# Optimization experiments

Hardware: AMD Instinct MI355X
Metric: run time of the kernel (lower is better)

The kernel has to match this reference:

```python
import jax, jax.numpy as jnp
import numpy as np

N_NODES = 5000
N_EDGES = 40000
BATCH = 4
SEQ = 12
IN_FEAT = 64
OUT_FEAT = 64


def setup_inputs() -> dict:
    key = jax.random.key(0)
    k1, k2, k3, k4 = jax.random.split(key, 4)
    features = jax.random.normal(k1, (N_NODES, BATCH, SEQ, IN_FEAT), dtype=jnp.float32)
    # glorot-uniform-like scale for the shared weight
    limit = np.sqrt(6.0 / (IN_FEAT + OUT_FEAT)).astype(np.float32)
    weight = jax.random.uniform(k2, (IN_FEAT, OUT_FEAT), dtype=jnp.float32,
                                minval=-limit, maxval=limit)
    edges_dst = jax.random.randint(k3, (N_EDGES,), 0, N_NODES, dtype=jnp.int32)
    edges_src = jax.random.randint(k4, (N_EDGES,), 0, N_NODES, dtype=jnp.int32)
    return {"features": features, "weight": weight,
            "edges_dst": edges_dst, "edges_src": edges_src}


def reference(features, weight, edges_dst, edges_src):
    num_nodes = features.shape[0]
    # nodes' own representation: (N, B, T, Fin) @ (Fin, Fout)
    nodes_rep = jnp.matmul(features, weight)
    # gather source-node features for every edge: (E, B, T, Fin)
    gathered = features[edges_src]
    # unsorted_segment_mean over destination nodes
    summed = jax.ops.segment_sum(gathered, edges_dst, num_segments=num_nodes)
    counts = jax.ops.segment_sum(jnp.ones((edges_dst.shape[0],), dtype=features.dtype),
                                 edges_dst, num_segments=num_nodes)
    mean = summed / jnp.maximum(counts, 1.0)[:, None, None, None]
    agg_messages = jnp.matmul(mean, weight)
    # combination_type = 'concat', activation = relu
    h = jnp.concatenate([nodes_rep, agg_messages], axis=-1)
    return jax.nn.relu(h)
```

## Files before the change

kernel.cpp:

```cpp
#include <hip/hip_runtime.h>

#define N_NODES 5000
#define N_EDGES 40000
#define ROWS 48
#define FIN 64
#define FOUT 64
#define NODE_ELEMS (ROWS * FIN)
#define OUT_ROW 128
#define NODE_OUT (ROWS * OUT_ROW)
#define CAP 64
#define M_ROWS (N_NODES * ROWS)

typedef float f32x4 __attribute__((ext_vector_type(4)));
typedef short bf16x8 __attribute__((ext_vector_type(8)));

__device__ __forceinline__ unsigned short f32_to_bf16_rne(float f) {
    unsigned int u = __float_as_uint(f);
    u += 0x7fffu + ((u >> 16) & 1u);
    return (unsigned short)(u >> 16);
}


__global__ void prep_kernel(const float* __restrict__ W,
                            int* __restrict__ counts,
                            unsigned short* __restrict__ Wt) {
    const int tid = threadIdx.x;
    if (blockIdx.x < 20) {
        int i = blockIdx.x * 256 + tid;
        if (i < N_NODES) counts[i] = 0;
    } else {
        int base = tid * 16;
        int j = base >> 6;
        int k0 = base & 63;
        ushort4 pk[4];
        #pragma unroll
        for (int q = 0; q < 4; ++q) {
            unsigned short p[4];
            #pragma unroll
            for (int m = 0; m < 4; ++m)
                p[m] = f32_to_bf16_rne(W[(k0 + q * 4 + m) * 64 + j]);
            pk[q].x = p[0]; pk[q].y = p[1]; pk[q].z = p[2]; pk[q].w = p[3];
        }
        #pragma unroll
        for (int q = 0; q < 4; ++q)
            *(ushort4*)(Wt + j * 64 + k0 + q * 4) = pk[q];
    }
}

__global__ void bucket_kernel(const int* __restrict__ edges_dst,
                              const int* __restrict__ edges_src,
                              int* __restrict__ counts,
                              int* __restrict__ bucket) {
    int e = blockIdx.x * 256 + threadIdx.x;
    if (e < N_EDGES) {
        int d = edges_dst[e];
        int slot = atomicAdd(&counts[d], 1);
        if (slot < CAP) bucket[d * CAP + slot] = edges_src[e];
    }
}


__global__ __launch_bounds__(256) void mfma_matmul_kernel(
    const float* __restrict__ feat,
    const unsigned short* __restrict__ Wt,
    float* __restrict__ out,
    unsigned short* __restrict__ Q) {
    __shared__ __align__(16) float c_lds[64 * 64];

    const int tid  = threadIdx.x;
    const int wave = tid >> 6;
    const int lane = tid & 63;
    const int row16 = lane & 15;
    const int koct  = lane >> 4;

    const size_t g0 = (size_t)blockIdx.x * 64;

    const float* arow = feat + (g0 + wave * 16 + row16) * FIN + koct * 8;
    f32x4 a00 = *(const f32x4*)(arow);
    f32x4 a01 = *(const f32x4*)(arow + 4);
    f32x4 a10 = *(const f32x4*)(arow + 32);
    f32x4 a11 = *(const f32x4*)(arow + 36);

    bf16x8 bfrag[2][4];
    #pragma unroll
    for (int t = 0; t < 4; ++t) {
        const unsigned short* wcol = Wt + (t * 16 + row16) * 64 + koct * 8;
        bfrag[0][t] = *(const bf16x8*)(wcol);
        bfrag[1][t] = *(const bf16x8*)(wcol + 32);
    }

    bf16x8 afrag[2];
    {
        unsigned short p[16];
        #pragma unroll
        for (int m = 0; m < 4; ++m) {
            p[m]      = f32_to_bf16_rne(a00[m]);
            p[4 + m]  = f32_to_bf16_rne(a01[m]);
            p[8 + m]  = f32_to_bf16_rne(a10[m]);
            p[12 + m] = f32_to_bf16_rne(a11[m]);
        }
        #pragma unroll
        for (int m = 0; m < 8; ++m) { afrag[0][m] = (short)p[m]; afrag[1][m] = (short)p[8 + m]; }
    }

    f32x4 acc[4];
    #pragma unroll
    for (int t = 0; t < 4; ++t) acc[t] = (f32x4){0.f, 0.f, 0.f, 0.f};

    #pragma unroll
    for (int s = 0; s < 2; ++s)
        #pragma unroll
        for (int t = 0; t < 4; ++t)
            acc[t] = __builtin_amdgcn_mfma_f32_16x16x32_bf16(afrag[s], bfrag[s][t], acc[t], 0, 0, 0);

    #pragma unroll
    for (int t = 0; t < 4; ++t)
        #pragma unroll
        for (int p = 0; p < 4; ++p)
            c_lds[(wave * 16 + koct * 4 + p) * 64 + t * 16 + row16] = acc[t][p];
    __syncthreads();

    #pragma unroll
    for (int i = 0; i < 4; ++i) {
        int c = tid + i * 256;
        int r = c >> 4;
        int cq = c & 15;
        f32x4 v = ((const f32x4*)c_lds)[c];
        f32x4 rv = {fmaxf(v.x, 0.f), fmaxf(v.y, 0.f), fmaxf(v.z, 0.f), fmaxf(v.w, 0.f)};
        *(f32x4*)(out + (g0 + r) * OUT_ROW + cq * 4) = rv;
    }
    #pragma unroll
    for (int i = 0; i < 2; ++i) {
        int c = tid + i * 256;
        int r = c >> 3;
        int part = c & 7;
        const float* src = c_lds + r * 64 + part * 8;
        ushort4 lo, hi;
        lo.x = f32_to_bf16_rne(src[0]); lo.y = f32_to_bf16_rne(src[1]);
        lo.z = f32_to_bf16_rne(src[2]); lo.w = f32_to_bf16_rne(src[3]);
        hi.x = f32_to_bf16_rne(src[4]); hi.y = f32_to_bf16_rne(src[5]);
        hi.z = f32_to_bf16_rne(src[6]); hi.w = f32_to_bf16_rne(src[7]);
        unsigned short* dst = Q + (g0 + r) * FIN + part * 8;
        *(ushort4*)(dst) = lo;
        *(ushort4*)(dst + 4) = hi;
    }
}


__device__ __forceinline__ void acc_u4(float* a, uint4 v) {
    a[0] += __uint_as_float(v.x << 16); a[1] += __uint_as_float(v.x & 0xffff0000u);
    a[2] += __uint_as_float(v.y << 16); a[3] += __uint_as_float(v.y & 0xffff0000u);
    a[4] += __uint_as_float(v.z << 16); a[5] += __uint_as_float(v.z & 0xffff0000u);
    a[6] += __uint_as_float(v.w << 16); a[7] += __uint_as_float(v.w & 0xffff0000u);
}

__global__ __launch_bounds__(384) void gather_kernel(
    const unsigned short* __restrict__ Q,
    const int* __restrict__ counts,
    const int* __restrict__ bucket,
    float* __restrict__ out) {
    const int n = blockIdx.x;
    const int tid = threadIdx.x;
    const int cnt_true = counts[n];
    const int cnt = cnt_true < CAP ? cnt_true : CAP;
    const int* bk = bucket + n * CAP;

    float acc[8];
    #pragma unroll
    for (int i = 0; i < 8; ++i) acc[i] = 0.f;

    int e = 0;
    for (; e + 4 <= cnt; e += 4) {
        const unsigned short* q0 = Q + (size_t)bk[e]     * NODE_ELEMS;
        const unsigned short* q1 = Q + (size_t)bk[e + 1] * NODE_ELEMS;
        const unsigned short* q2 = Q + (size_t)bk[e + 2] * NODE_ELEMS;
        const unsigned short* q3 = Q + (size_t)bk[e + 3] * NODE_ELEMS;
        uint4 a0 = *(const uint4*)(q0 + tid * 8);
        uint4 a1 = *(const uint4*)(q1 + tid * 8);
        uint4 a2 = *(const uint4*)(q2 + tid * 8);
        uint4 a3 = *(const uint4*)(q3 + tid * 8);
        acc_u4(acc, a0); acc_u4(acc, a1); acc_u4(acc, a2); acc_u4(acc, a3);
    }
    for (; e < cnt; ++e) {
        const unsigned short* q0 = Q + (size_t)bk[e] * NODE_ELEMS;
        uint4 a0 = *(const uint4*)(q0 + tid * 8);
        acc_u4(acc, a0);
    }

    const float inv = 1.0f / (float)(cnt_true > 1 ? cnt_true : 1);
    float* outn = out + (size_t)n * NODE_OUT;

    int r = tid >> 3, c = (tid & 7) * 8;
    float* p = outn + r * OUT_ROW + 64 + c;
    f32x4 v0 = {fmaxf(acc[0] * inv, 0.f), fmaxf(acc[1] * inv, 0.f),
                fmaxf(acc[2] * inv, 0.f), fmaxf(acc[3] * inv, 0.f)};
    f32x4 v1 = {fmaxf(acc[4] * inv, 0.f), fmaxf(acc[5] * inv, 0.f),
                fmaxf(acc[6] * inv, 0.f), fmaxf(acc[7] * inv, 0.f)};
    *(f32x4*)(p)     = v0;
    *(f32x4*)(p + 4) = v1;
}


__global__ void zero_counts_kernel(int* __restrict__ counts) {
    int i = blockIdx.x * 256 + threadIdx.x;
    if (i < N_NODES) counts[i] = 0;
}

__global__ void hist_kernel(const int* __restrict__ edges_dst, int* __restrict__ counts) {
    int e = blockIdx.x * 256 + threadIdx.x;
    if (e < N_EDGES) atomicAdd(&counts[edges_dst[e]], 1);
}

__global__ void scan_kernel(const int* __restrict__ counts,
                            int* __restrict__ offsets,
                            int* __restrict__ cursor) {
    __shared__ int buf[1024];
    __shared__ int carry_s;
    int tid = threadIdx.x;
    if (tid == 0) carry_s = 0;
    __syncthreads();
    for (int base = 0; base < N_NODES; base += 1024) {
        int i = base + tid;
        int v = (i < N_NODES) ? counts[i] : 0;
        buf[tid] = v;
        __syncthreads();
        int x = v;
        for (int off = 1; off < 1024; off <<= 1) {
            int t = (tid >= off) ? buf[tid - off] : 0;
            __syncthreads();
            x += t;
            buf[tid] = x;
            __syncthreads();
        }
        int c = carry_s;
        if (i < N_NODES) {
            int excl = c + x - v;
            offsets[i] = excl;
            cursor[i] = excl;
        }
        __syncthreads();
        if (tid == 0) carry_s = c + buf[1023];
        __syncthreads();
    }
    if (threadIdx.x == 0) offsets[N_NODES] = carry_s;
}

__global__ void scatter_kernel(const int* __restrict__ edges_dst,
                               const int* __restrict__ edges_src,
                               int* __restrict__ cursor,
                               int* __restrict__ csr_src) {
    int e = blockIdx.x * 256 + threadIdx.x;
    if (e < N_EDGES) {
        int d = edges_dst[e];
        int p = atomicAdd(&cursor[d], 1);
        csr_src[p] = edges_src[e];
    }
}

__global__ __launch_bounds__(256) void fused_kernel(
    const float* __restrict__ feat,
    const float* __restrict__ W,
    const int* __restrict__ offsets,
    const int* __restrict__ csr_src,
    float* __restrict__ out) {
    __shared__ __align__(16) float lds_w[FIN * FOUT];
    __shared__ __align__(16) float lds_t[NODE_ELEMS];

    const int n = blockIdx.x;
    const int tid = threadIdx.x;

    {
        const f32x4* w4 = (const f32x4*)W;
        f32x4* l4 = (f32x4*)lds_w;
        #pragma unroll
        for (int i = 0; i < 4; ++i) l4[tid + i * 256] = w4[tid + i * 256];
    }
    {
        const f32x4* f4 = (const f32x4*)(feat + (size_t)n * NODE_ELEMS);
        f32x4* l4 = (f32x4*)lds_t;
        #pragma unroll
        for (int i = 0; i < 3; ++i) l4[tid + i * 256] = f4[tid + i * 256];
    }
    __syncthreads();

    const int j = tid & 63;
    float wcol[64];
    #pragma unroll
    for (int k = 0; k < 64; ++k) wcol[k] = lds_w[k * 64 + j];

    float* outn = out + (size_t)n * NODE_OUT;

    #pragma unroll
    for (int i = 0; i < 12; ++i) {
        int r = (tid + i * 256) >> 6;
        const f32x4* m4 = (const f32x4*)(lds_t + r * 64);
        float s = 0.f;
        #pragma unroll
        for (int k4 = 0; k4 < 16; ++k4) {
            f32x4 m = m4[k4];
            s += m.x * wcol[4 * k4 + 0] + m.y * wcol[4 * k4 + 1] +
                 m.z * wcol[4 * k4 + 2] + m.w * wcol[4 * k4 + 3];
        }
        outn[r * OUT_ROW + j] = fmaxf(s, 0.f);
    }

    const int e0 = offsets[n], e1 = offsets[n + 1];
    f32x4 acc[3];
    #pragma unroll
    for (int i = 0; i < 3; ++i) acc[i] = (f32x4){0.f, 0.f, 0.f, 0.f};
    for (int e = e0; e < e1; ++e) {
        int src = csr_src[e];
        const f32x4* f4 = (const f32x4*)(feat + (size_t)src * NODE_ELEMS);
        #pragma unroll
        for (int i = 0; i < 3; ++i) acc[i] += f4[tid + i * 256];
    }
    const float inv = 1.0f / (float)((e1 - e0) > 1 ? (e1 - e0) : 1);

    __syncthreads();
    {
        f32x4* l4 = (f32x4*)lds_t;
        #pragma unroll
        for (int i = 0; i < 3; ++i) l4[tid + i * 256] = acc[i] * inv;
    }
    __syncthreads();

    #pragma unroll
    for (int i = 0; i < 12; ++i) {
        int r = (tid + i * 256) >> 6;
        const f32x4* m4 = (const f32x4*)(lds_t + r * 64);
        float s = 0.f;
        #pragma unroll
        for (int k4 = 0; k4 < 16; ++k4) {
            f32x4 m = m4[k4];
            s += m.x * wcol[4 * k4 + 0] + m.y * wcol[4 * k4 + 1] +
                 m.z * wcol[4 * k4 + 2] + m.w * wcol[4 * k4 + 3];
        }
        outn[r * OUT_ROW + 64 + j] = fmaxf(s, 0.f);
    }
}


extern "C" void kernel_launch(void* const* d_in, const int* in_sizes, int n_in,
                              void* d_out, int out_size, void* d_ws, size_t ws_size,
                              hipStream_t stream) {
    const float* feat = (const float*)d_in[0];
    const float* W    = (const float*)d_in[1];
    const int* edst   = (const int*)d_in[2];
    const int* esrc   = (const int*)d_in[3];
    float* out = (float*)d_out;

    int* counts  = (int*)d_ws;
    int* bucket  = (int*)((char*)d_ws + 20480);
    const size_t wt_off = 20480 + (size_t)N_NODES * CAP * 4;
    unsigned short* Wt = (unsigned short*)((char*)d_ws + wt_off);
    const size_t q_off = wt_off + 8192;
    unsigned short* Q = (unsigned short*)((char*)d_ws + q_off);
    const size_t q_bytes = (size_t)N_NODES * NODE_ELEMS * 2;

    if (ws_size >= q_off + q_bytes) {
        prep_kernel<<<21, 256, 0, stream>>>(W, counts, Wt);
        bucket_kernel<<<(N_EDGES + 255) / 256, 256, 0, stream>>>(edst, esrc, counts, bucket);
        mfma_matmul_kernel<<<M_ROWS / 64, 256, 0, stream>>>(feat, Wt, out, Q);
        gather_kernel<<<N_NODES, 384, 0, stream>>>(Q, counts, bucket, out);
    } else {
        int* offsets = counts + N_NODES;
        int* cursor  = offsets + N_NODES + 1;
        int* csr_src = cursor + N_NODES;
        zero_counts_kernel<<<(N_NODES + 255) / 256, 256, 0, stream>>>(counts);
        hist_kernel<<<(N_EDGES + 255) / 256, 256, 0, stream>>>(edst, counts);
        scan_kernel<<<1, 1024, 0, stream>>>(counts, offsets, cursor);
        scatter_kernel<<<(N_EDGES + 255) / 256, 256, 0, stream>>>(edst, esrc, cursor, csr_src);
        fused_kernel<<<N_NODES, 256, 0, stream>>>(feat, W, offsets, csr_src, out);
    }
}
```

Baseline: 82.16 us.

## Merge bucket and weight-prep kernels, memset counts, split gather across two blocks

Replaces the prep kernel's zeroing of counts with a hipMemsetAsync. The edge bucketing and the bf16 weight transpose now run in one kernel, which cuts one launch. The gather kernel now uses two 192-thread blocks per node, each covering half of the node's rows, instead of one 384-thread block. This doubles the block count for better occupancy but reads the bucket list twice. The scalar tail loop becomes unrolled 2+1 steps.

```diff
diff --git a/kernel.cpp b/kernel.cpp
--- a/kernel.cpp
+++ b/kernel.cpp
@@ -10,6 +10,7 @@
 #define NODE_OUT (ROWS * OUT_ROW)
 #define CAP 64
 #define M_ROWS (N_NODES * ROWS)
+#define EDGE_BLOCKS ((N_EDGES + 255) / 256)
 
 typedef float f32x4 __attribute__((ext_vector_type(4)));
 typedef short bf16x8 __attribute__((ext_vector_type(8)));
@@ -21,41 +22,33 @@
 }
 
 
-__global__ void prep_kernel(const float* __restrict__ W,
-                            int* __restrict__ counts,
-                            unsigned short* __restrict__ Wt) {
+__global__ void bucket_wt_kernel(const int* __restrict__ edges_dst,
+                                 const int* __restrict__ edges_src,
+                                 const float* __restrict__ W,
+                                 int* __restrict__ counts,
+                                 int* __restrict__ bucket,
+                                 unsigned short* __restrict__ Wt) {
     const int tid = threadIdx.x;
-    if (blockIdx.x < 20) {
-        int i = blockIdx.x * 256 + tid;
-        if (i < N_NODES) counts[i] = 0;
+    if (blockIdx.x < EDGE_BLOCKS) {
+        int e = blockIdx.x * 256 + tid;
+        if (e < N_EDGES) {
+            int d = edges_dst[e];
+            int slot = atomicAdd(&counts[d], 1);
+            if (slot < CAP) bucket[d * CAP + slot] = edges_src[e];
+        }
     } else {
         int base = tid * 16;
         int j = base >> 6;
         int k0 = base & 63;
-        ushort4 pk[4];
         #pragma unroll
         for (int q = 0; q < 4; ++q) {
-            unsigned short p[4];
-            #pragma unroll
-            for (int m = 0; m < 4; ++m)
-                p[m] = f32_to_bf16_rne(W[(k0 + q * 4 + m) * 64 + j]);
-            pk[q].x = p[0]; pk[q].y = p[1]; pk[q].z = p[2]; pk[q].w = p[3];
-        }
-        #pragma unroll
-        for (int q = 0; q < 4; ++q)
-            *(ushort4*)(Wt + j * 64 + k0 + q * 4) = pk[q];
-    }
-}
-
-__global__ void bucket_kernel(const int* __restrict__ edges_dst,
-                              const int* __restrict__ edges_src,
-                              int* __restrict__ counts,
-                              int* __restrict__ bucket) {
-    int e = blockIdx.x * 256 + threadIdx.x;
-    if (e < N_EDGES) {
-        int d = edges_dst[e];
-        int slot = atomicAdd(&counts[d], 1);
-        if (slot < CAP) bucket[d * CAP + slot] = edges_src[e];
+            ushort4 pk;
+            pk.x = f32_to_bf16_rne(W[(k0 + q * 4 + 0) * 64 + j]);
+            pk.y = f32_to_bf16_rne(W[(k0 + q * 4 + 1) * 64 + j]);
+            pk.z = f32_to_bf16_rne(W[(k0 + q * 4 + 2) * 64 + j]);
+            pk.w = f32_to_bf16_rne(W[(k0 + q * 4 + 3) * 64 + j]);
+            *(ushort4*)(Wt + j * 64 + k0 + q * 4) = pk;
+        }
     }
 }
 
@@ -154,13 +147,15 @@
     a[6] += __uint_as_float(v.w << 16); a[7] += __uint_as_float(v.w & 0xffff0000u);
 }
 
-__global__ __launch_bounds__(384) void gather_kernel(
+__global__ __launch_bounds__(192) void gather_kernel(
     const unsigned short* __restrict__ Q,
     const int* __restrict__ counts,
     const int* __restrict__ bucket,
     float* __restrict__ out) {
-    const int n = blockIdx.x;
+    const int n = blockIdx.x >> 1;
+    const int half = blockIdx.x & 1;
     const int tid = threadIdx.x;
+    const int elem0 = half * 1536 + tid * 8;
     const int cnt_true = counts[n];
     const int cnt = cnt_true < CAP ? cnt_true : CAP;
     const int* bk = bucket + n * CAP;
@@ -171,27 +166,33 @@
 
     int e = 0;
     for (; e + 4 <= cnt; e += 4) {
-        const unsigned short* q0 = Q + (size_t)bk[e]     * NODE_ELEMS;
-        const unsigned short* q1 = Q + (size_t)bk[e + 1] * NODE_ELEMS;
-        const unsigned short* q2 = Q + (size_t)bk[e + 2] * NODE_ELEMS;
-        const unsigned short* q3 = Q + (size_t)bk[e + 3] * NODE_ELEMS;
-        uint4 a0 = *(const uint4*)(q0 + tid * 8);
-        uint4 a1 = *(const uint4*)(q1 + tid * 8);
-        uint4 a2 = *(const uint4*)(q2 + tid * 8);
-        uint4 a3 = *(const uint4*)(q3 + tid * 8);
+        const unsigned short* q0 = Q + (size_t)bk[e]     * NODE_ELEMS + elem0;
+        const unsigned short* q1 = Q + (size_t)bk[e + 1] * NODE_ELEMS + elem0;
+        const unsigned short* q2 = Q + (size_t)bk[e + 2] * NODE_ELEMS + elem0;
+        const unsigned short* q3 = Q + (size_t)bk[e + 3] * NODE_ELEMS + elem0;
+        uint4 a0 = *(const uint4*)(q0);
+        uint4 a1 = *(const uint4*)(q1);
+        uint4 a2 = *(const uint4*)(q2);
+        uint4 a3 = *(const uint4*)(q3);
         acc_u4(acc, a0); acc_u4(acc, a1); acc_u4(acc, a2); acc_u4(acc, a3);
     }
-    for (; e < cnt; ++e) {
-        const unsigned short* q0 = Q + (size_t)bk[e] * NODE_ELEMS;
-        uint4 a0 = *(const uint4*)(q0 + tid * 8);
+    if (e + 2 <= cnt) {
+        const unsigned short* q0 = Q + (size_t)bk[e]     * NODE_ELEMS + elem0;
+        const unsigned short* q1 = Q + (size_t)bk[e + 1] * NODE_ELEMS + elem0;
+        uint4 a0 = *(const uint4*)(q0);
+        uint4 a1 = *(const uint4*)(q1);
+        acc_u4(acc, a0); acc_u4(acc, a1);
+        e += 2;
+    }
+    if (e < cnt) {
+        const unsigned short* q0 = Q + (size_t)bk[e] * NODE_ELEMS + elem0;
+        uint4 a0 = *(const uint4*)(q0);
         acc_u4(acc, a0);
     }
 
     const float inv = 1.0f / (float)(cnt_true > 1 ? cnt_true : 1);
-    float* outn = out + (size_t)n * NODE_OUT;
-
-    int r = tid >> 3, c = (tid & 7) * 8;
-    float* p = outn + r * OUT_ROW + 64 + c;
+    int r = elem0 >> 6, c = elem0 & 63;
+    float* p = out + (size_t)n * NODE_OUT + r * OUT_ROW + 64 + c;
     f32x4 v0 = {fmaxf(acc[0] * inv, 0.f), fmaxf(acc[1] * inv, 0.f),
                 fmaxf(acc[2] * inv, 0.f), fmaxf(acc[3] * inv, 0.f)};
     f32x4 v1 = {fmaxf(acc[4] * inv, 0.f), fmaxf(acc[5] * inv, 0.f),
@@ -358,10 +359,10 @@
     const size_t q_bytes = (size_t)N_NODES * NODE_ELEMS * 2;
 
     if (ws_size >= q_off + q_bytes) {
-        prep_kernel<<<21, 256, 0, stream>>>(W, counts, Wt);
-        bucket_kernel<<<(N_EDGES + 255) / 256, 256, 0, stream>>>(edst, esrc, counts, bucket);
+        hipMemsetAsync(counts, 0, N_NODES * sizeof(int), stream);
+        bucket_wt_kernel<<<EDGE_BLOCKS + 1, 256, 0, stream>>>(edst, esrc, W, counts, bucket, Wt);
         mfma_matmul_kernel<<<M_ROWS / 64, 256, 0, stream>>>(feat, Wt, out, Q);
-        gather_kernel<<<N_NODES, 384, 0, stream>>>(Q, counts, bucket, out);
+        gather_kernel<<<N_NODES * 2, 192, 0, stream>>>(Q, counts, bucket, out);
     } else {
         int* offsets = counts + N_NODES;
         int* cursor  = offsets + N_NODES + 1;
```

After: 78.56 us. 4.4% less time.
